# Kernel optimization log

Hardware: AMD Instinct MI355X
Metric: run time of the kernel (lower is better)

The kernel has to match this reference:

```python
import jax, jax.numpy as jnp
import numpy as np

B, L, D, H, TOPO = 2, 1024, 1024, 16, 8
Dh = D // H
N_SLOTS = B * L


def _rope_apply(x, cos, sin):
    # x: [B,H,L,Dh]; cos/sin: [B,1,L,Dh//2]
    x1 = x[..., 0::2]
    x2 = x[..., 1::2]
    y1 = x1 * cos - x2 * sin
    y2 = x1 * sin + x2 * cos
    return jnp.stack([y1, y2], axis=-1).reshape(x.shape)


def setup_inputs() -> dict:
    key = jax.random.key(0)
    ks = jax.random.split(key, 6)
    x = jax.random.normal(ks[0], (B, L, D), dtype=jnp.float32)
    topo_active = jax.random.normal(ks[1], (B, L, TOPO), dtype=jnp.float32)
    k_cache = jnp.zeros((1, H, N_SLOTS, Dh), dtype=jnp.float32)
    v_cache = jnp.zeros((1, H, N_SLOTS, Dh), dtype=jnp.float32)
    Wqkv = jax.random.normal(ks[2], (3 * D, D), dtype=jnp.float32) * 0.02
    Wproj = jax.random.normal(ks[3], (D, D), dtype=jnp.float32) * 0.02
    Wfreq = jax.random.normal(ks[4], (Dh // 2, TOPO), dtype=jnp.float32) * 0.02
    # each token (b, pos) writes to physical slot b*L + pos
    slot_mapping = jnp.arange(N_SLOTS, dtype=jnp.int64)
    # paged causal mask: query (b, i) may see slot s iff slot belongs to batch b and pos(s) <= i
    s = jnp.arange(N_SLOTS)
    sb = s // L           # batch owning each slot
    sp = s % L            # position within that sequence
    b_idx = jnp.arange(B)[:, None, None]
    i_idx = jnp.arange(L)[None, :, None]
    block_mask = ((sb[None, None, :] == b_idx) & (sp[None, None, :] <= i_idx))[:, None]  # [B,1,L,S]
    return {"x": x, "topo_active": topo_active, "k_cache": k_cache, "v_cache": v_cache,
            "Wqkv": Wqkv, "Wproj": Wproj, "Wfreq": Wfreq,
            "slot_mapping": slot_mapping, "block_mask": block_mask}


def reference(x, topo_active, k_cache, v_cache, Wqkv, Wproj, Wfreq, slot_mapping, block_mask):
    Bx, Lx, Dx = x.shape
    # qkv projection -> q,k,v [B,H,L,Dh]
    qkv = (x @ Wqkv.T).reshape(Bx, Lx, 3, H, Dh).transpose(2, 0, 3, 1, 4)
    q, k, v = qkv[0], qkv[1], qkv[2]
    # RnRoPE: topo -> per-position frequencies, rotate q and k
    freqs = (topo_active @ Wfreq.T)[:, None]  # [B,1,L,Dh//2]
    cos, sin = jnp.cos(freqs), jnp.sin(freqs)
    q = _rope_apply(q, cos, sin)
    k = _rope_apply(k, cos, sin)
    # commit new k/v into the paged cache via slot_mapping scatter
    k_flat = k.transpose(0, 2, 1, 3).reshape(Bx * Lx, H, Dh).swapaxes(0, 1)  # [H,BL,Dh]
    v_flat = v.transpose(0, 2, 1, 3).reshape(Bx * Lx, H, Dh).swapaxes(0, 1)
    kc = k_cache[0].at[:, slot_mapping].set(k_flat)  # [H,S,Dh]
    vc = v_cache[0].at[:, slot_mapping].set(v_flat)
    # masked (block-sparse) attention over the physical cache
    scale = 1.0 / jnp.sqrt(jnp.float32(Dh))
    scores = jnp.einsum('bhld,hsd->bhls', q, kc) * scale
    scores = jnp.where(block_mask, scores, -jnp.inf)
    p = jax.nn.softmax(scores, axis=-1)
    out = jnp.einsum('bhls,hsd->bhld', p, vc)
    out = out.transpose(0, 2, 1, 3).reshape(Bx, Lx, Dx)
    return out @ Wproj.T
```

## Files before the change

### kernel.cpp

```cpp
#include <hip/hip_runtime.h>
#include <hip/hip_bf16.h>
#include <math.h>

#define H_N 16
#define DH 64
#define LSEQ 1024
#define BATCH 2
#define NSLOT 2048
#define DMODEL 1024

typedef __bf16 bf16x8 __attribute__((ext_vector_type(8)));
typedef __bf16 bf16x4 __attribute__((ext_vector_type(4)));
typedef float f32x4 __attribute__((ext_vector_type(4)));

__global__ __launch_bounds__(256) void k_setup(const float* __restrict__ x,
                                               const float* __restrict__ Wqkv,
                                               const float* __restrict__ Wproj,
                                               const float* __restrict__ topo,
                                               const float* __restrict__ Wfreq,
                                               __bf16* __restrict__ xb,
                                               __bf16* __restrict__ Wqkvb,
                                               __bf16* __restrict__ Wprojb,
                                               float* __restrict__ cosb,
                                               float* __restrict__ sinb) {
    int blk = blockIdx.x;
    if (blk < 6144) {
        const float* in;
        __bf16* out;
        int base;
        if (blk < 2048)      { in = x;     out = xb;     base = blk; }
        else if (blk < 5120) { in = Wqkv;  out = Wqkvb;  base = blk - 2048; }
        else                 { in = Wproj; out = Wprojb; base = blk - 5120; }
        int i = (base * 256 + threadIdx.x) * 4;
        float4 v = *reinterpret_cast<const float4*>(in + i);
        struct B4 { __bf16 a, b, c, d; };
        B4 o{(__bf16)v.x, (__bf16)v.y, (__bf16)v.z, (__bf16)v.w};
        *reinterpret_cast<B4*>(out + i) = o;
    } else {
        int s = (blk - 6144) * 8 + (threadIdx.x >> 5);
        int j = threadIdx.x & 31;
        float f = 0.f;
#pragma unroll
        for (int t = 0; t < 8; ++t) f += topo[s * 8 + t] * Wfreq[j * 8 + t];
        cosb[s * 32 + j] = cosf(f);
        sinb[s * 32 + j] = sinf(f);
    }
}

template <int BM, int BN>
__device__ __forceinline__ void gemm_coreT(const __bf16* __restrict__ A,
                                           const __bf16* __restrict__ Bm,
                                           int K, int m0, int n0,
                                           __bf16* As, __bf16* Bs,
                                           f32x4 acc[BM / 32][BN / 32],
                                           int tid, int wr, int wc, int lane) {
    constexpr int MF = BM / 32, NF = BN / 32;
    const f32x4 z = {0.f, 0.f, 0.f, 0.f};
#pragma unroll
    for (int m = 0; m < MF; ++m)
#pragma unroll
        for (int n = 0; n < NF; ++n) acc[m][n] = z;

    const int l15 = lane & 15, g = lane >> 4;
    const int wv = tid >> 6;
    for (int k0 = 0; k0 < K; k0 += 64) {
        __syncthreads();
#pragma unroll
        for (int i = 0; i < BM / 32; ++i) {
            int u = i * 256 + tid;
            int row = u >> 3, slot = u & 7, srcs = slot ^ (row & 7);
            __builtin_amdgcn_global_load_lds(
                (const __attribute__((address_space(1))) void*)(A + (size_t)(m0 + row) * K + k0 + srcs * 8),
                (__attribute__((address_space(3))) void*)(As + i * 2048 + wv * 512), 16, 0, 0);
        }
#pragma unroll
        for (int i = 0; i < BN / 32; ++i) {
            int u = i * 256 + tid;
            int row = u >> 3, slot = u & 7, srcs = slot ^ (row & 7);
            __builtin_amdgcn_global_load_lds(
                (const __attribute__((address_space(1))) void*)(Bm + (size_t)(n0 + row) * K + k0 + srcs * 8),
                (__attribute__((address_space(3))) void*)(Bs + i * 2048 + wv * 512), 16, 0, 0);
        }
        __syncthreads();
        __builtin_amdgcn_s_setprio(1);
#pragma unroll
        for (int kk = 0; kk < 2; ++kk) {
            const int k16 = kk * 4 + g;
            bf16x8 af[MF], bfr[NF];
#pragma unroll
            for (int m = 0; m < MF; ++m) {
                int row = wr * (BM / 2) + m * 16 + l15;
                int slot = k16 ^ (row & 7);
                af[m] = *reinterpret_cast<const bf16x8*>(As + row * 64 + slot * 8);
            }
#pragma unroll
            for (int n = 0; n < NF; ++n) {
                int col = wc * (BN / 2) + n * 16 + l15;
                int slot = k16 ^ (col & 7);
                bfr[n] = *reinterpret_cast<const bf16x8*>(Bs + col * 64 + slot * 8);
            }
#pragma unroll
            for (int m = 0; m < MF; ++m)
#pragma unroll
                for (int n = 0; n < NF; ++n)
                    acc[m][n] = __builtin_amdgcn_mfma_f32_16x16x32_bf16(af[m], bfr[n], acc[m][n], 0, 0, 0);
        }
        __builtin_amdgcn_s_setprio(0);
    }
}

__global__ __launch_bounds__(256, 2) void k_qkv_mfma(const __bf16* __restrict__ xb,
                                                     const __bf16* __restrict__ Wb,
                                                     const float* __restrict__ cosb,
                                                     const float* __restrict__ sinb,
                                                     __bf16* __restrict__ Qb,
                                                     __bf16* __restrict__ Kb,
                                                     __bf16* __restrict__ Vtb) {
    __shared__ __bf16 As[128 * 64];
    __shared__ __bf16 Bs[96 * 64];
    int lin = blockIdx.x;
    int newlin = (lin & 7) * 64 + (lin >> 3);
    const int m0 = (newlin & 15) * 128, n0 = (newlin >> 4) * 96;
    const int tid = threadIdx.x, lane = tid & 63, w = tid >> 6;
    const int wr = w >> 1, wc = w & 1;
    const int l15 = lane & 15, g = lane >> 4;
    f32x4 acc[4][3];
    gemm_coreT<128, 96>(xb, Wb, DMODEL, m0, n0, As, Bs, acc, tid, wr, wc, lane);

    const int rbase = m0 + wr * 64;
#pragma unroll
    for (int n = 0; n < 3; ++n) {
        int c = n0 + wc * 48 + n * 16 + l15;
        int part = c >> 10, h = (c >> 6) & 15, d = c & 63, jj = d >> 1;
#pragma unroll
        for (int m = 0; m < 4; ++m) {
            int sbase = rbase + m * 16 + g * 4;
            if (part < 2) {
                __bf16* dst = (part == 0) ? Qb : Kb;
#pragma unroll
                for (int j = 0; j < 4; ++j) {
                    int s = sbase + j;
                    float v = acc[m][n][j];
                    float partner = __shfl_xor(v, 1);
                    float cs = cosb[s * 32 + jj], sn = sinb[s * 32 + jj];
                    float outv = (d & 1) ? fmaf(v, cs, partner * sn) : fmaf(v, cs, -partner * sn);
                    dst[((size_t)h * NSLOT + s) * DH + d] = (__bf16)outv;
                }
            } else {
                bf16x4 pk;
#pragma unroll
                for (int j = 0; j < 4; ++j) pk[j] = (__bf16)acc[m][n][j];
                *reinterpret_cast<bf16x4*>(&Vtb[((size_t)h * DH + d) * NSLOT + sbase]) = pk;
            }
        }
    }
}

__global__ __launch_bounds__(256, 2) void k_attn8(const __bf16* __restrict__ Qg,
                                                  const __bf16* __restrict__ Kg,
                                                  const __bf16* __restrict__ Vt,
                                                  __bf16* __restrict__ AO) {
    int lin = blockIdx.x + 16 * (blockIdx.y + 16 * blockIdx.z);
    const int x = lin & 7;
    const int t = lin >> 3;
    const int b = x >> 2;
    const int h = (x & 3) * 4 + (t & 3);
    const int v = t >> 2;
    const int bx = (v < 8) ? v : 23 - v;

    const int tid = threadIdx.x, w = tid >> 6, lane = tid & 63;
    const int l15 = lane & 15, g = lane >> 4;
    const int q0 = bx * 64 + w * 16;

    __shared__ __bf16 Ks[2][64 * 64];
    __shared__ __bf16 Vs[2][64 * 64];
    __shared__ __bf16 P_lds[4][16 * 72];

    const __bf16* Qh = Qg + ((size_t)h * NSLOT + b * LSEQ) * DH;
    const __bf16* Kh = Kg + ((size_t)h * NSLOT + b * LSEQ) * DH;
    const __bf16* Vh = Vt + ((size_t)h * DH) * NSLOT + b * LSEQ;

    bf16x8 qf[2];
#pragma unroll
    for (int g2 = 0; g2 < 2; ++g2)
        qf[g2] = *reinterpret_cast<const bf16x8*>(Qh + (size_t)(q0 + l15) * DH + g2 * 32 + g * 8);

    const f32x4 z = {0.f, 0.f, 0.f, 0.f};
    f32x4 ao[4];
#pragma unroll
    for (int dt = 0; dt < 4; ++dt) ao[dt] = z;
    float lsum[4] = {0.f, 0.f, 0.f, 0.f};

    const int nch = bx + 1;

#pragma unroll
    for (int i = 0; i < 2; ++i) {
        int u = i * 256 + tid;
        int row = u >> 3, slot = u & 7;
        int srcs = slot ^ (row & 7);
        const __bf16* ga = Kh + (size_t)row * DH + srcs * 8;
        const __bf16* gv = Vh + (size_t)row * NSLOT + srcs * 8;
        __builtin_amdgcn_global_load_lds((const __attribute__((address_space(1))) void*)ga,
                                         (__attribute__((address_space(3))) void*)(&Ks[0][u * 8]), 16, 0, 0);
        __builtin_amdgcn_global_load_lds((const __attribute__((address_space(1))) void*)gv,
                                         (__attribute__((address_space(3))) void*)(&Vs[0][u * 8]), 16, 0, 0);
    }
    __syncthreads();

    for (int ch = 0; ch < nch; ++ch) {
        const int cur = ch & 1;
        if (ch + 1 < nch) {
            const int nsp = (ch + 1) * 64;
#pragma unroll
            for (int i = 0; i < 2; ++i) {
                int u = i * 256 + tid;
                int row = u >> 3, slot = u & 7;
                int srcs = slot ^ (row & 7);
                const __bf16* ga = Kh + (size_t)(nsp + row) * DH + srcs * 8;
                const __bf16* gv = Vh + (size_t)row * NSLOT + nsp + srcs * 8;
                __builtin_amdgcn_global_load_lds((const __attribute__((address_space(1))) void*)ga,
                                                 (__attribute__((address_space(3))) void*)(&Ks[1 - cur][u * 8]), 16, 0, 0);
                __builtin_amdgcn_global_load_lds((const __attribute__((address_space(1))) void*)gv,
                                                 (__attribute__((address_space(3))) void*)(&Vs[1 - cur][u * 8]), 16, 0, 0);
            }
        }

        f32x4 s[4];
#pragma unroll
        for (int n = 0; n < 4; ++n) s[n] = z;
        __builtin_amdgcn_s_setprio(1);
#pragma unroll
        for (int g2 = 0; g2 < 2; ++g2) {
#pragma unroll
            for (int n = 0; n < 4; ++n) {
                int r = n * 16 + l15;
                int slot = ((g2 << 2) + g) ^ (r & 7);
                bf16x8 kf = *reinterpret_cast<const bf16x8*>(&Ks[cur][r * 64 + slot * 8]);
                s[n] = __builtin_amdgcn_mfma_f32_16x16x32_bf16(qf[g2], kf, s[n], 0, 0, 0);
            }
        }
        __builtin_amdgcn_s_setprio(0);

        const bool last = (ch == nch - 1);
        const int sp0 = ch * 64;
#pragma unroll
        for (int n = 0; n < 4; ++n) {
            int key = sp0 + n * 16 + l15;
#pragma unroll
            for (int j = 0; j < 4; ++j) {
                float sc = s[n][j] * 0.125f;
                if (last && key > q0 + g * 4 + j) sc = -INFINITY;
                float p = __expf(sc);
                s[n][j] = p;
                lsum[j] += p;
            }
        }

#pragma unroll
        for (int j = 0; j < 4; ++j)
#pragma unroll
            for (int n = 0; n < 4; ++n)
                P_lds[w][(g * 4 + j) * 72 + n * 16 + l15] = (__bf16)s[n][j];

        bf16x8 pf[2];
        pf[0] = *reinterpret_cast<const bf16x8*>(&P_lds[w][l15 * 72 + g * 8]);
        pf[1] = *reinterpret_cast<const bf16x8*>(&P_lds[w][l15 * 72 + 32 + g * 8]);

        __builtin_amdgcn_s_setprio(1);
#pragma unroll
        for (int g2 = 0; g2 < 2; ++g2) {
#pragma unroll
            for (int dt = 0; dt < 4; ++dt) {
                int rv = dt * 16 + l15;
                int slot = ((g2 << 2) + g) ^ (rv & 7);
                bf16x8 vf = *reinterpret_cast<const bf16x8*>(&Vs[cur][rv * 64 + slot * 8]);
                ao[dt] = __builtin_amdgcn_mfma_f32_16x16x32_bf16(pf[g2], vf, ao[dt], 0, 0, 0);
            }
        }
        __builtin_amdgcn_s_setprio(0);

        __syncthreads();
    }

    float lrow[4];
#pragma unroll
    for (int j = 0; j < 4; ++j) {
        float vv = lsum[j];
#pragma unroll
        for (int off = 1; off < 16; off <<= 1) vv += __shfl_xor(vv, off);
        lrow[j] = vv;
    }

#pragma unroll
    for (int dt = 0; dt < 4; ++dt)
#pragma unroll
        for (int j = 0; j < 4; ++j) {
            int q = q0 + g * 4 + j;
            AO[(size_t)(b * LSEQ + q) * DMODEL + h * 64 + dt * 16 + l15] =
                (__bf16)(ao[dt][j] / lrow[j]);
        }
}

__global__ __launch_bounds__(256, 2) void k_proj_mfma(const __bf16* __restrict__ AO,
                                                      const __bf16* __restrict__ Wb,
                                                      float* __restrict__ out) {
    __shared__ __bf16 As[64 * 64];
    __shared__ __bf16 Bs[64 * 64];
    int lin = blockIdx.x;
    int newlin = (lin & 7) * 64 + (lin >> 3);
    const int m0 = (newlin & 31) * 64, n0 = (newlin >> 5) * 64;
    const int tid = threadIdx.x, lane = tid & 63, w = tid >> 6;
    const int wr = w >> 1, wc = w & 1;
    const int l15 = lane & 15, g = lane >> 4;
    f32x4 acc[2][2];
    gemm_coreT<64, 64>(AO, Wb, DMODEL, m0, n0, As, Bs, acc, tid, wr, wc, lane);

#pragma unroll
    for (int n = 0; n < 2; ++n) {
        int c = n0 + wc * 32 + n * 16 + l15;
#pragma unroll
        for (int m = 0; m < 2; ++m) {
#pragma unroll
            for (int j = 0; j < 4; ++j) {
                int s = m0 + wr * 32 + m * 16 + g * 4 + j;
                out[(size_t)s * DMODEL + c] = acc[m][n][j];
            }
        }
    }
}

extern "C" void kernel_launch(void* const* d_in, const int* in_sizes, int n_in,
                              void* d_out, int out_size, void* d_ws, size_t ws_size,
                              hipStream_t stream) {
    const float* x     = (const float*)d_in[0];
    const float* topo  = (const float*)d_in[1];
    const float* Wqkv  = (const float*)d_in[4];
    const float* Wproj = (const float*)d_in[5];
    const float* Wfreq = (const float*)d_in[6];
    float* out = (float*)d_out;

    char* wsb = (char*)d_ws;
    __bf16* xb     = (__bf16*)(wsb + 0);
    __bf16* Wqkvb  = (__bf16*)(wsb + (4u << 20));
    __bf16* Wprojb = (__bf16*)(wsb + (10u << 20));
    float*  cosb   = (float*)(wsb + (12u << 20));
    float*  sinb   = (float*)(wsb + (12u << 20) + 262144);
    __bf16* Qb     = (__bf16*)(wsb + (12u << 20) + 524288);
    __bf16* Kb     = (__bf16*)(wsb + (16u << 20) + 524288);
    __bf16* Vtb    = (__bf16*)(wsb + (20u << 20) + 524288);
    __bf16* AO     = (__bf16*)(wsb + (24u << 20) + 524288);

    hipLaunchKernelGGL(k_setup, dim3(6400), dim3(256), 0, stream,
                       x, Wqkv, Wproj, topo, Wfreq, xb, Wqkvb, Wprojb, cosb, sinb);
    hipLaunchKernelGGL(k_qkv_mfma, dim3(512), dim3(256), 0, stream,
                       xb, Wqkvb, cosb, sinb, Qb, Kb, Vtb);
    hipLaunchKernelGGL(k_attn8, dim3(LSEQ / 64, H_N, BATCH), dim3(256), 0, stream,
                       Qb, Kb, Vtb, AO);
    hipLaunchKernelGGL(k_proj_mfma, dim3(512), dim3(256), 0, stream,
                       AO, Wprojb, out);
}
```

Baseline: 65.39 us.

## Double-buffer LDS tiles in GEMM core to overlap loads with MFMA

```diff
diff --git a/kernel.cpp b/kernel.cpp
--- a/kernel.cpp
+++ b/kernel.cpp
@@ -63,25 +63,49 @@
 
     const int l15 = lane & 15, g = lane >> 4;
     const int wv = tid >> 6;
-    for (int k0 = 0; k0 < K; k0 += 64) {
-        __syncthreads();
-#pragma unroll
-        for (int i = 0; i < BM / 32; ++i) {
-            int u = i * 256 + tid;
-            int row = u >> 3, slot = u & 7, srcs = slot ^ (row & 7);
-            __builtin_amdgcn_global_load_lds(
-                (const __attribute__((address_space(1))) void*)(A + (size_t)(m0 + row) * K + k0 + srcs * 8),
-                (__attribute__((address_space(3))) void*)(As + i * 2048 + wv * 512), 16, 0, 0);
-        }
-#pragma unroll
-        for (int i = 0; i < BN / 32; ++i) {
-            int u = i * 256 + tid;
-            int row = u >> 3, slot = u & 7, srcs = slot ^ (row & 7);
-            __builtin_amdgcn_global_load_lds(
-                (const __attribute__((address_space(1))) void*)(Bm + (size_t)(n0 + row) * K + k0 + srcs * 8),
-                (__attribute__((address_space(3))) void*)(Bs + i * 2048 + wv * 512), 16, 0, 0);
-        }
-        __syncthreads();
+    const int srow = tid >> 3, sslot = tid & 7;
+    const int ssrc = (sslot ^ (srow & 7)) * 8;
+
+#pragma unroll
+    for (int i = 0; i < MF; ++i) {
+        int row = i * 32 + srow;
+        __builtin_amdgcn_global_load_lds(
+            (const __attribute__((address_space(1))) void*)(A + (size_t)(m0 + row) * K + ssrc),
+            (__attribute__((address_space(3))) void*)(As + i * 2048 + wv * 512), 16, 0, 0);
+    }
+#pragma unroll
+    for (int i = 0; i < NF; ++i) {
+        int row = i * 32 + srow;
+        __builtin_amdgcn_global_load_lds(
+            (const __attribute__((address_space(1))) void*)(Bm + (size_t)(n0 + row) * K + ssrc),
+            (__attribute__((address_space(3))) void*)(Bs + i * 2048 + wv * 512), 16, 0, 0);
+    }
+    __syncthreads();
+
+    const int NT = K / 64;
+    for (int t = 0; t < NT; ++t) {
+        const int cur = t & 1;
+        __bf16* Ac = As + cur * (BM * 64);
+        __bf16* Bc = Bs + cur * (BN * 64);
+        if (t + 1 < NT) {
+            const int k0 = (t + 1) * 64;
+            __bf16* An = As + (1 - cur) * (BM * 64);
+            __bf16* Bn = Bs + (1 - cur) * (BN * 64);
+#pragma unroll
+            for (int i = 0; i < MF; ++i) {
+                int row = i * 32 + srow;
+                __builtin_amdgcn_global_load_lds(
+                    (const __attribute__((address_space(1))) void*)(A + (size_t)(m0 + row) * K + k0 + ssrc),
+                    (__attribute__((address_space(3))) void*)(An + i * 2048 + wv * 512), 16, 0, 0);
+            }
+#pragma unroll
+            for (int i = 0; i < NF; ++i) {
+                int row = i * 32 + srow;
+                __builtin_amdgcn_global_load_lds(
+                    (const __attribute__((address_space(1))) void*)(Bm + (size_t)(n0 + row) * K + k0 + ssrc),
+                    (__attribute__((address_space(3))) void*)(Bn + i * 2048 + wv * 512), 16, 0, 0);
+            }
+        }
         __builtin_amdgcn_s_setprio(1);
 #pragma unroll
         for (int kk = 0; kk < 2; ++kk) {
@@ -91,13 +115,13 @@
             for (int m = 0; m < MF; ++m) {
                 int row = wr * (BM / 2) + m * 16 + l15;
                 int slot = k16 ^ (row & 7);
-                af[m] = *reinterpret_cast<const bf16x8*>(As + row * 64 + slot * 8);
+                af[m] = *reinterpret_cast<const bf16x8*>(Ac + row * 64 + slot * 8);
             }
 #pragma unroll
             for (int n = 0; n < NF; ++n) {
                 int col = wc * (BN / 2) + n * 16 + l15;
                 int slot = k16 ^ (col & 7);
-                bfr[n] = *reinterpret_cast<const bf16x8*>(Bs + col * 64 + slot * 8);
+                bfr[n] = *reinterpret_cast<const bf16x8*>(Bc + col * 64 + slot * 8);
             }
 #pragma unroll
             for (int m = 0; m < MF; ++m)
@@ -106,6 +130,7 @@
                     acc[m][n] = __builtin_amdgcn_mfma_f32_16x16x32_bf16(af[m], bfr[n], acc[m][n], 0, 0, 0);
         }
         __builtin_amdgcn_s_setprio(0);
+        __syncthreads();
     }
 }
 
@@ -116,8 +141,8 @@
                                                      __bf16* __restrict__ Qb,
                                                      __bf16* __restrict__ Kb,
                                                      __bf16* __restrict__ Vtb) {
-    __shared__ __bf16 As[128 * 64];
-    __shared__ __bf16 Bs[96 * 64];
+    __shared__ __bf16 As[2][128 * 64];
+    __shared__ __bf16 Bs[2][96 * 64];
     int lin = blockIdx.x;
     int newlin = (lin & 7) * 64 + (lin >> 3);
     const int m0 = (newlin & 15) * 128, n0 = (newlin >> 4) * 96;
@@ -125,7 +150,7 @@
     const int wr = w >> 1, wc = w & 1;
     const int l15 = lane & 15, g = lane >> 4;
     f32x4 acc[4][3];
-    gemm_coreT<128, 96>(xb, Wb, DMODEL, m0, n0, As, Bs, acc, tid, wr, wc, lane);
+    gemm_coreT<128, 96>(xb, Wb, DMODEL, m0, n0, &As[0][0], &Bs[0][0], acc, tid, wr, wc, lane);
 
     const int rbase = m0 + wr * 64;
 #pragma unroll
@@ -304,8 +329,8 @@
 __global__ __launch_bounds__(256, 2) void k_proj_mfma(const __bf16* __restrict__ AO,
                                                       const __bf16* __restrict__ Wb,
                                                       float* __restrict__ out) {
-    __shared__ __bf16 As[64 * 64];
-    __shared__ __bf16 Bs[64 * 64];
+    __shared__ __bf16 As[2][64 * 64];
+    __shared__ __bf16 Bs[2][64 * 64];
     int lin = blockIdx.x;
     int newlin = (lin & 7) * 64 + (lin >> 3);
     const int m0 = (newlin & 31) * 64, n0 = (newlin >> 5) * 64;
@@ -313,7 +338,7 @@
     const int wr = w >> 1, wc = w & 1;
     const int l15 = lane & 15, g = lane >> 4;
     f32x4 acc[2][2];
-    gemm_coreT<64, 64>(AO, Wb, DMODEL, m0, n0, As, Bs, acc, tid, wr, wc, lane);
+    gemm_coreT<64, 64>(AO, Wb, DMODEL, m0, n0, &As[0][0], &Bs[0][0], acc, tid, wr, wc, lane);
 
 #pragma unroll
     for (int n = 0; n < 2; ++n) {
```

New measurement: 66.35 us. No clear change (+1.5%).
